# Optimization experiments

Measured on AMD Instinct MI355X. Metric: run time of the kernel, lower is better.

The kernel has to match this reference:

```python
import jax, jax.numpy as jnp
import numpy as np

N_NODES = 50000
N_EDGES = 800000
IN_CH, HIDDEN, OUT_CH = 64, 16, 8


def setup_inputs() -> dict:
    key = jax.random.key(0)
    ks = jax.random.split(key, 8)
    x = jax.random.normal(ks[0], (N_NODES, IN_CH), dtype=jnp.float32)
    edge_index = jax.random.randint(ks[1], (2, N_EDGES), 0, N_NODES, dtype=jnp.int64)
    # SAGEConv params: lin_l (neighbor aggregate, has bias), lin_r (root, no bias)
    s1 = 1.0 / np.sqrt(IN_CH)
    s2 = 1.0 / np.sqrt(HIDDEN)
    W1l = jax.random.uniform(ks[2], (HIDDEN, IN_CH), jnp.float32, -s1, s1)
    W1r = jax.random.uniform(ks[3], (HIDDEN, IN_CH), jnp.float32, -s1, s1)
    b1 = jax.random.uniform(ks[4], (HIDDEN,), jnp.float32, -s1, s1)
    W2l = jax.random.uniform(ks[5], (OUT_CH, HIDDEN), jnp.float32, -s2, s2)
    W2r = jax.random.uniform(ks[6], (OUT_CH, HIDDEN), jnp.float32, -s2, s2)
    b2 = jax.random.uniform(ks[7], (OUT_CH,), jnp.float32, -s2, s2)
    return {"x": x, "W1l": W1l, "W1r": W1r, "b1": b1,
            "W2l": W2l, "W2r": W2r, "b2": b2, "edge_index": edge_index}


def _sage_conv(x, src, dst, Wl, Wr, b, n_nodes):
    # mean-aggregate neighbor features: gather from src, scatter-mean to dst
    msg_sum = jax.ops.segment_sum(x[src], dst, num_segments=n_nodes)  # [N, d]
    deg = jax.ops.segment_sum(jnp.ones((src.shape[0], 1), x.dtype), dst,
                              num_segments=n_nodes)                    # [N, 1]
    aggr = msg_sum / jnp.maximum(deg, 1.0)
    # out = lin_l(aggr) + lin_r(x); bias lives in lin_l
    return aggr @ Wl.T + x @ Wr.T + b


def reference(x, W1l, W1r, b1, W2l, W2r, b2, edge_index):
    src, dst = edge_index[0], edge_index[1]
    n = x.shape[0]
    h = jax.nn.relu(_sage_conv(x, src, dst, W1l, W1r, b1, n))
    # F.dropout(p=0.1, training=self.training): identity in eval mode
    return _sage_conv(h, src, dst, W2l, W2r, b2, n)
```

## Files before the change

### kernel.cpp

```cpp
#include <hip/hip_runtime.h>

#define IN_CH 64
#define HID   16
#define OUTC  8
#define BINSHIFT 6
#define BINCAP  (1 << BINSHIFT)

#define CHUNK_A     2048
#define SLICE_SHIFT 6
#define SLICE_NODES 64
#define SUBWORDS    16

typedef _Float16 half2_t __attribute__((ext_vector_type(2)));
typedef _Float16 half8_t __attribute__((ext_vector_type(8)));


__global__ __launch_bounds__(256) void build_xform(
    const float* __restrict__ x,
    const int*   __restrict__ esrc,
    const int*   __restrict__ edst,
    const float* __restrict__ W1l,
    const float* __restrict__ W1r,
    const float* __restrict__ b1,
    unsigned int* __restrict__ gbuf,
    _Float16* __restrict__ y1h,
    float* __restrict__ r1,
    int n_nodes, int n_edges, int nb_part, int nsl)
{
    __shared__ __align__(16) char smem[53248];

    int b   = blockIdx.x;
    int tid = threadIdx.x;

    if (b < nb_part) {
        int* scurs = (int*)smem;
        unsigned* sline = (unsigned*)(smem + 3200);
        for (int i = tid; i < nsl; i += 256) scurs[i] = 0;
        __syncthreads();
        int base = b * CHUNK_A;
#pragma unroll
        for (int j = 0; j < CHUNK_A / 256; ++j) {
            int e = base + j * 256 + tid;
            if (e < n_edges) {
                int d  = edst[e];
                int s  = esrc[e];
                int bk = d >> SLICE_SHIFT;
                int pos = atomicAdd(&scurs[bk], 1);
                if (pos < SUBWORDS - 1)
                    sline[(bk << 4) + 1 + pos] =
                        (unsigned)s |
                        ((unsigned)(d & (SLICE_NODES - 1)) << 16);
            }
        }
        __syncthreads();
        for (int i = tid; i < nsl; i += 256) {
            int c = scurs[i];
            sline[i << 4] = c > SUBWORDS - 1 ? SUBWORDS - 1 : c;
        }
        __syncthreads();
        for (int i = tid; i < (nsl << 2); i += 256) {
            int sl = i >> 2, w4 = i & 3;
            *(uint4*)(gbuf + ((size_t)sl * nb_part + b) * SUBWORDS + (w4 << 2)) =
                *(const uint4*)&sline[(sl << 4) + (w4 << 2)];
        }
        return;
    }

    float* sWl = (float*)smem;
    float* sWr = (float*)(smem + 4352);
    float* sx  = (float*)(smem + 8704);
    float* sb1 = (float*)(smem + 13056);
    for (int i = tid; i < HID * IN_CH; i += 256) {
        int c = i >> 6, k = i & 63;
        sWl[c * 68 + k] = W1l[i];
        sWr[c * 68 + k] = W1r[i];
    }
    if (tid < HID) sb1[tid] = b1[tid];

    int nl = tid >> 4;
    int c  = tid & 15;
    int base_node = (b - nb_part) * 64;
#pragma unroll
    for (int sb = 0; sb < 4; ++sb) {
        int node = base_node + sb * 16 + nl;
        __syncthreads();
        if (node < n_nodes)
            *(float4*)&sx[nl * 68 + c * 4] =
                *(const float4*)&x[(size_t)node * IN_CH + c * 4];
        __syncthreads();
        if (node < n_nodes) {
            float accL = 0.f, accR = 0.f;
#pragma unroll
            for (int k4 = 0; k4 < 16; ++k4) {
                float4 xv = *(const float4*)&sx [nl * 68 + k4 * 4];
                float4 wl = *(const float4*)&sWl[c  * 68 + k4 * 4];
                float4 wr = *(const float4*)&sWr[c  * 68 + k4 * 4];
                accL = fmaf(xv.x, wl.x, accL); accL = fmaf(xv.y, wl.y, accL);
                accL = fmaf(xv.z, wl.z, accL); accL = fmaf(xv.w, wl.w, accL);
                accR = fmaf(xv.x, wr.x, accR); accR = fmaf(xv.y, wr.y, accR);
                accR = fmaf(xv.z, wr.z, accR); accR = fmaf(xv.w, wr.w, accR);
            }
            y1h[(size_t)node * HID + c] = (_Float16)accL;
            r1 [(size_t)node * HID + c] = accR + sb1[c];
        }
    }
}

#define ACC8(v)                                                          \
    do {                                                                 \
        half2_t p01 = {(v).s0, (v).s1}, p23 = {(v).s2, (v).s3};          \
        half2_t p45 = {(v).s4, (v).s5}, p67 = {(v).s6, (v).s7};          \
        s0 = __builtin_amdgcn_fdot2(p01, k10, s0, false);                \
        s1 = __builtin_amdgcn_fdot2(p01, k01, s1, false);                \
        s2 = __builtin_amdgcn_fdot2(p23, k10, s2, false);                \
        s3 = __builtin_amdgcn_fdot2(p23, k01, s3, false);                \
        s4 = __builtin_amdgcn_fdot2(p45, k10, s4, false);                \
        s5 = __builtin_amdgcn_fdot2(p45, k01, s5, false);                \
        s6 = __builtin_amdgcn_fdot2(p67, k10, s6, false);                \
        s7 = __builtin_amdgcn_fdot2(p67, k01, s7, false);                \
    } while (0)

#define EMIT(pw)                                                         \
    do {                                                                 \
        unsigned pp = (pw);                                              \
        int dl  = pp >> 16;                                              \
        int pos = atomicAdd(&scnt[dl], 1);                               \
        if (pos < BINCAP) bins[(dl << BINSHIFT) + pos] = (unsigned short)pp; \
    } while (0)

__global__ __launch_bounds__(256) void slice_gather(
    const float* __restrict__ r1,
    const _Float16* __restrict__ y1h,
    const unsigned int* __restrict__ gbuf,
    const float* __restrict__ W2l, const float* __restrict__ W2r,
    const float* __restrict__ b2,
    int* __restrict__ cur,
    unsigned short* __restrict__ adj,
    _Float16* __restrict__ y2h, float* __restrict__ out,
    int n_nodes, int nb_part)
{
    __shared__ int scnt[SLICE_NODES];
    __shared__ __align__(16) unsigned short bins[SLICE_NODES * BINCAP];
    __shared__ float sW2l[HID * OUTC];
    __shared__ float sW2r[HID * OUTC];
    __shared__ float sb2[OUTC];
    __shared__ float sh[32 * 17];

    int b   = blockIdx.x;
    int tid = threadIdx.x;

    for (int i = tid; i < HID * OUTC; i += 256) {
        int o = i >> 4, k = i & 15;
        sW2l[k * OUTC + o] = W2l[i];
        sW2r[k * OUTC + o] = W2r[i];
    }
    if (tid < OUTC) sb2[tid] = b2[tid];
    if (tid < SLICE_NODES) scnt[tid] = 0;
    __syncthreads();

    for (int a = tid; a < nb_part; a += 256) {
        const unsigned int* lp = gbuf + ((size_t)b * nb_part + a) * SUBWORDS;
        uint4 q0 = *(const uint4*)lp;
        int cnt = (int)q0.x;
        if (cnt > 0) EMIT(q0.y);
        if (cnt > 1) EMIT(q0.z);
        if (cnt > 2) EMIT(q0.w);
        if (cnt > 3) {
            uint4 q1 = *(const uint4*)(lp + 4);
            EMIT(q1.x);
            if (cnt > 4) EMIT(q1.y);
            if (cnt > 5) EMIT(q1.z);
            if (cnt > 6) EMIT(q1.w);
            if (cnt > 7) {
                uint4 q2 = *(const uint4*)(lp + 8);
                EMIT(q2.x);
                if (cnt > 8)  EMIT(q2.y);
                if (cnt > 9)  EMIT(q2.z);
                if (cnt > 10) EMIT(q2.w);
                if (cnt > 11) {
                    uint4 q3 = *(const uint4*)(lp + 12);
                    EMIT(q3.x);
                    if (cnt > 12) EMIT(q3.y);
                    if (cnt > 13) EMIT(q3.z);
                    if (cnt > 14) EMIT(q3.w);
                }
            }
        }
    }
    __syncthreads();

    int node0  = b << SLICE_SHIFT;
    int nvalid = n_nodes - node0;
    if (nvalid > SLICE_NODES) nvalid = SLICE_NODES;
    if (nvalid < 0) nvalid = 0;

    if (tid < nvalid) cur[node0 + tid] = scnt[tid];
    int nv = nvalid << 3;
    for (int i = tid; i < nv; i += 256)
        *(uint4*)(adj + ((size_t)node0 << BINSHIFT) + ((size_t)i << 3)) =
            *(const uint4*)&bins[(size_t)i << 3];

    int nl = tid >> 3;
    int t  = tid & 7;
    int h  = t >> 2;
    int ep = t & 3;

    const half2_t k10 = {(_Float16)1.f, (_Float16)0.f};
    const half2_t k01 = {(_Float16)0.f, (_Float16)1.f};

#pragma unroll
    for (int batch = 0; batch < SLICE_NODES / 32; ++batch) {
        __syncthreads();
        int ln   = batch * 32 + nl;
        int node = node0 + ln;
        bool real = ln < nvalid;
        if (real) {
            int deg = scnt[ln];
            if (deg > BINCAP) deg = BINCAP;
            int iters = deg >> 2;
            float s0 = 0.f, s1 = 0.f, s2 = 0.f, s3 = 0.f;
            float s4 = 0.f, s5 = 0.f, s6 = 0.f, s7 = 0.f;
            const _Float16* yq = y1h + h * 8;
            const unsigned short* row = &bins[ln << BINSHIFT];
            for (int it = ep; it < iters; it += 4) {
                ushort4 s = *(const ushort4*)(row + (it << 2));
                half8_t v0 = *(const half8_t*)(yq + (size_t)s.x * HID);
                half8_t v1 = *(const half8_t*)(yq + (size_t)s.y * HID);
                half8_t v2 = *(const half8_t*)(yq + (size_t)s.z * HID);
                half8_t v3 = *(const half8_t*)(yq + (size_t)s.w * HID);
                ACC8(v0); ACC8(v1); ACC8(v2); ACC8(v3);
            }
            for (int g = (iters << 2) + ep; g < deg; g += 4) {
                half8_t v = *(const half8_t*)(yq + (size_t)row[g] * HID);
                ACC8(v);
            }
            s0 += __shfl_xor(s0, 1); s0 += __shfl_xor(s0, 2);
            s1 += __shfl_xor(s1, 1); s1 += __shfl_xor(s1, 2);
            s2 += __shfl_xor(s2, 1); s2 += __shfl_xor(s2, 2);
            s3 += __shfl_xor(s3, 1); s3 += __shfl_xor(s3, 2);
            s4 += __shfl_xor(s4, 1); s4 += __shfl_xor(s4, 2);
            s5 += __shfl_xor(s5, 1); s5 += __shfl_xor(s5, 2);
            s6 += __shfl_xor(s6, 1); s6 += __shfl_xor(s6, 2);
            s7 += __shfl_xor(s7, 1); s7 += __shfl_xor(s7, 2);
            if (ep == 0) {
                float inv = 1.0f / fmaxf((float)deg, 1.0f);
                const float* rr = &r1[(size_t)node * HID + h * 8];
                float4 ra = *(const float4*)(rr);
                float4 rb = *(const float4*)(rr + 4);
                float* shp = &sh[nl * 17 + h * 8];
                shp[0] = fmaxf(fmaf(s0, inv, ra.x), 0.f);
                shp[1] = fmaxf(fmaf(s1, inv, ra.y), 0.f);
                shp[2] = fmaxf(fmaf(s2, inv, ra.z), 0.f);
                shp[3] = fmaxf(fmaf(s3, inv, ra.w), 0.f);
                shp[4] = fmaxf(fmaf(s4, inv, rb.x), 0.f);
                shp[5] = fmaxf(fmaf(s5, inv, rb.y), 0.f);
                shp[6] = fmaxf(fmaf(s6, inv, rb.z), 0.f);
                shp[7] = fmaxf(fmaf(s7, inv, rb.w), 0.f);
            }
        }
        __syncthreads();
        if (real) {
            const float* hrow = &sh[nl * 17];
            float al = 0.f, ar = sb2[t];
#pragma unroll
            for (int k = 0; k < HID; ++k) {
                float hv = hrow[k];
                al = fmaf(hv, sW2l[k * OUTC + t], al);
                ar = fmaf(hv, sW2r[k * OUTC + t], ar);
            }
            y2h[(size_t)node * OUTC + t] = (_Float16)al;
            out[(size_t)node * OUTC + t] = ar;
        }
    }
}

__global__ __launch_bounds__(256) void gather_out(
    const _Float16* __restrict__ y2h,
    const int*   __restrict__ cur,
    const unsigned short* __restrict__ adj,
    float* __restrict__ out,
    int n_nodes)
{
    int tid  = threadIdx.x;
    int node = blockIdx.x * 64 + (tid >> 2);
    if (node >= n_nodes) return;
    int ep = tid & 3;

    int deg = cur[node];
    if (deg > BINCAP) deg = BINCAP;
    int iters = deg >> 2;
    const unsigned short* row = adj + ((size_t)node << BINSHIFT);
    const ushort4* ap = (const ushort4*)row;

    const half2_t k10 = {(_Float16)1.f, (_Float16)0.f};
    const half2_t k01 = {(_Float16)0.f, (_Float16)1.f};

    float s0 = 0.f, s1 = 0.f, s2 = 0.f, s3 = 0.f;
    float s4 = 0.f, s5 = 0.f, s6 = 0.f, s7 = 0.f;
    for (int it = ep; it < iters; it += 4) {
        ushort4 s = ap[it];
        half8_t v0 = *(const half8_t*)(y2h + (size_t)s.x * OUTC);
        half8_t v1 = *(const half8_t*)(y2h + (size_t)s.y * OUTC);
        half8_t v2 = *(const half8_t*)(y2h + (size_t)s.z * OUTC);
        half8_t v3 = *(const half8_t*)(y2h + (size_t)s.w * OUTC);
        ACC8(v0); ACC8(v1); ACC8(v2); ACC8(v3);
    }
    for (int g = (iters << 2) + ep; g < deg; g += 4) {
        half8_t v = *(const half8_t*)(y2h + (size_t)row[g] * OUTC);
        ACC8(v);
    }
    s0 += __shfl_xor(s0, 1); s0 += __shfl_xor(s0, 2);
    s1 += __shfl_xor(s1, 1); s1 += __shfl_xor(s1, 2);
    s2 += __shfl_xor(s2, 1); s2 += __shfl_xor(s2, 2);
    s3 += __shfl_xor(s3, 1); s3 += __shfl_xor(s3, 2);
    s4 += __shfl_xor(s4, 1); s4 += __shfl_xor(s4, 2);
    s5 += __shfl_xor(s5, 1); s5 += __shfl_xor(s5, 2);
    s6 += __shfl_xor(s6, 1); s6 += __shfl_xor(s6, 2);
    s7 += __shfl_xor(s7, 1); s7 += __shfl_xor(s7, 2);
    if (ep != 0) return;

    float inv = 1.0f / fmaxf((float)deg, 1.0f);
    float* op = out + (size_t)node * OUTC;
    float4 c0 = *(float4*)op;
    float4 c1 = *(float4*)(op + 4);
    c0.x = fmaf(s0, inv, c0.x); c0.y = fmaf(s1, inv, c0.y);
    c0.z = fmaf(s2, inv, c0.z); c0.w = fmaf(s3, inv, c0.w);
    c1.x = fmaf(s4, inv, c1.x); c1.y = fmaf(s5, inv, c1.y);
    c1.z = fmaf(s6, inv, c1.z); c1.w = fmaf(s7, inv, c1.w);
    *(float4*)op = c0;
    *(float4*)(op + 4) = c1;
}

extern "C" void kernel_launch(void* const* d_in, const int* in_sizes, int n_in,
                              void* d_out, int out_size, void* d_ws, size_t ws_size,
                              hipStream_t stream)
{
    const float* x   = (const float*)d_in[0];
    const float* W1l = (const float*)d_in[1];
    const float* W1r = (const float*)d_in[2];
    const float* b1  = (const float*)d_in[3];
    const float* W2l = (const float*)d_in[4];
    const float* W2r = (const float*)d_in[5];
    const float* b2  = (const float*)d_in[6];
    const int*   ei  = (const int*)d_in[7];

    int n_nodes = in_sizes[0] / IN_CH;
    int n_edges = in_sizes[7] / 2;
    const int* esrc = ei;
    const int* edst = ei + n_edges;

    float* out = (float*)d_out;

    int nb_part = (n_edges + CHUNK_A - 1) / CHUNK_A;
    int nsl     = (n_nodes + SLICE_NODES - 1) >> SLICE_SHIFT;
    int nb_node = (n_nodes + 63) / 64;

    char* wsb = (char*)d_ws;
    _Float16* y1h = (_Float16*)wsb;
    _Float16* y2h = y1h + (size_t)n_nodes * HID;
    float* r1 = (float*)(y2h + (size_t)n_nodes * OUTC);
    int* cur  = (int*)(r1 + (size_t)n_nodes * HID);
    unsigned short* adj = (unsigned short*)(cur + n_nodes);
    unsigned int* gbuf = (unsigned int*)(adj + ((size_t)n_nodes << BINSHIFT));

    dim3 blk(256);

    build_xform<<<dim3(nb_part + nb_node), blk, 0, stream>>>(
        x, esrc, edst, W1l, W1r, b1, gbuf, y1h, r1,
        n_nodes, n_edges, nb_part, nsl);

    slice_gather<<<dim3(nsl), blk, 0, stream>>>(
        r1, y1h, gbuf, W2l, W2r, b2, cur, adj, y2h, out,
        n_nodes, nb_part);

    gather_out<<<dim3((n_nodes + 63) / 64), blk, 0, stream>>>(
        y2h, cur, adj, out, n_nodes);
}
```

Before: 113.1 us.

## Compact per-slice adjacency lists with packed offset/degree for gather_out

Replaces the fixed 64-slot-per-node adjacency array with a compacted per-slice layout. A serial prefix sum over the slice's node degrees (each rounded up to 4) fixes each node's offset. Offset and clamped degree are packed into one 32-bit word per node. This cuts the bytes written in slice_gather and read in gather_out, and improves locality. The cost is a single-thread serial scan and an extra barrier per block, and it assumes each slice's edges fit in SLICE_CAP (1536) entries.

```diff
diff --git a/kernel.cpp b/kernel.cpp
--- a/kernel.cpp
+++ b/kernel.cpp
@@ -10,6 +10,8 @@
 #define SLICE_SHIFT 6
 #define SLICE_NODES 64
 #define SUBWORDS    16
+
+#define SLICE_CAP   1536
 
 typedef _Float16 half2_t __attribute__((ext_vector_type(2)));
 typedef _Float16 half8_t __attribute__((ext_vector_type(8)));
@@ -134,12 +136,13 @@
     const unsigned int* __restrict__ gbuf,
     const float* __restrict__ W2l, const float* __restrict__ W2r,
     const float* __restrict__ b2,
-    int* __restrict__ cur,
-    unsigned short* __restrict__ adj,
+    unsigned int* __restrict__ off_deg,
+    unsigned short* __restrict__ adj_c,
     _Float16* __restrict__ y2h, float* __restrict__ out,
     int n_nodes, int nb_part)
 {
     __shared__ int scnt[SLICE_NODES];
+    __shared__ int soff[SLICE_NODES];
     __shared__ __align__(16) unsigned short bins[SLICE_NODES * BINCAP];
     __shared__ float sW2l[HID * OUTC];
     __shared__ float sW2r[HID * OUTC];
@@ -194,11 +197,31 @@
     if (nvalid > SLICE_NODES) nvalid = SLICE_NODES;
     if (nvalid < 0) nvalid = 0;
 
-    if (tid < nvalid) cur[node0 + tid] = scnt[tid];
-    int nv = nvalid << 3;
-    for (int i = tid; i < nv; i += 256)
-        *(uint4*)(adj + ((size_t)node0 << BINSHIFT) + ((size_t)i << 3)) =
-            *(const uint4*)&bins[(size_t)i << 3];
+    if (tid == 0) {
+        int acc = 0;
+        for (int i = 0; i < SLICE_NODES; ++i) {
+            soff[i] = acc;
+            int d = scnt[i]; if (d > BINCAP) d = BINCAP;
+            acc += (d + 3) & ~3;
+        }
+    }
+    __syncthreads();
+
+    if (tid < nvalid) {
+        int d = scnt[tid]; if (d > BINCAP) d = BINCAP;
+        off_deg[node0 + tid] = (unsigned)soff[tid] | ((unsigned)d << 16);
+    }
+    {
+        int ln = tid >> 2, q = tid & 3;
+        if (ln < nvalid) {
+            int d = scnt[ln]; if (d > BINCAP) d = BINCAP;
+            int nchunk = (d + 3) >> 2;
+            unsigned short* dst = adj_c + (size_t)b * SLICE_CAP + soff[ln];
+            const unsigned short* srcp = &bins[ln << BINSHIFT];
+            for (int j = q; j < nchunk; j += 4)
+                *(ushort4*)(dst + (j << 2)) = *(const ushort4*)(srcp + (j << 2));
+        }
+    }
 
     int nl = tid >> 3;
     int t  = tid & 7;
@@ -276,8 +299,8 @@
 
 __global__ __launch_bounds__(256) void gather_out(
     const _Float16* __restrict__ y2h,
-    const int*   __restrict__ cur,
-    const unsigned short* __restrict__ adj,
+    const unsigned int* __restrict__ off_deg,
+    const unsigned short* __restrict__ adj_c,
     float* __restrict__ out,
     int n_nodes)
 {
@@ -286,10 +309,11 @@
     if (node >= n_nodes) return;
     int ep = tid & 3;
 
-    int deg = cur[node];
-    if (deg > BINCAP) deg = BINCAP;
+    unsigned od = off_deg[node];
+    int deg = (int)(od >> 16);
+    const unsigned short* row =
+        adj_c + (size_t)(node >> SLICE_SHIFT) * SLICE_CAP + (od & 0xFFFF);
     int iters = deg >> 2;
-    const unsigned short* row = adj + ((size_t)node << BINSHIFT);
     const ushort4* ap = (const ushort4*)row;
 
     const half2_t k10 = {(_Float16)1.f, (_Float16)0.f};
@@ -359,9 +383,9 @@
     _Float16* y1h = (_Float16*)wsb;
     _Float16* y2h = y1h + (size_t)n_nodes * HID;
     float* r1 = (float*)(y2h + (size_t)n_nodes * OUTC);
-    int* cur  = (int*)(r1 + (size_t)n_nodes * HID);
-    unsigned short* adj = (unsigned short*)(cur + n_nodes);
-    unsigned int* gbuf = (unsigned int*)(adj + ((size_t)n_nodes << BINSHIFT));
+    unsigned int* off_deg = (unsigned int*)(r1 + (size_t)n_nodes * HID);
+    unsigned short* adj_c = (unsigned short*)(off_deg + n_nodes);
+    unsigned int* gbuf = (unsigned int*)(adj_c + (size_t)nsl * SLICE_CAP);
 
     dim3 blk(256);
 
@@ -370,9 +394,9 @@
         n_nodes, n_edges, nb_part, nsl);
 
     slice_gather<<<dim3(nsl), blk, 0, stream>>>(
-        r1, y1h, gbuf, W2l, W2r, b2, cur, adj, y2h, out,
+        r1, y1h, gbuf, W2l, W2r, b2, off_deg, adj_c, y2h, out,
         n_nodes, nb_part);
 
     gather_out<<<dim3((n_nodes + 63) / 64), blk, 0, stream>>>(
-        y2h, cur, adj, out, n_nodes);
+        y2h, off_deg, adj_c, out, n_nodes);
 }
```

After: 112.3 us. No clear change (-0.7%).
